# Kernel optimization log

Measured on AMD Instinct MI355X. Metric: run time of the kernel, lower is better.

## Reference

```python
import jax, jax.numpy as jnp
import numpy as np

B, N, E, H = 4, 512, 256, 8
D = E // H


def setup_inputs() -> dict:
    key = jax.random.key(0)
    ks = jax.random.split(key, 14)
    s = 1.0 / np.sqrt(E)
    inp = {
        "query": jax.random.normal(ks[0], (B, N, E), jnp.float32),
        "attn_bias": jax.random.normal(ks[1], (B * H, N, N), jnp.float32),
        "delta_pos": jax.random.normal(ks[2], (B, N, N, 3), jnp.float32),
        "drop_edge_mask": jax.random.bernoulli(ks[3], 0.1, (N, N)),
        "Wq": jax.random.normal(ks[4], (E, E), jnp.float32) * s,
        "bq": jnp.zeros((E,), jnp.float32),
        "Wk": jax.random.normal(ks[5], (E, E), jnp.float32) * s,
        "bk": jnp.zeros((E,), jnp.float32),
        "Wv": jax.random.normal(ks[6], (E, E), jnp.float32) * s,
        "bv": jnp.zeros((E,), jnp.float32),
        "Wf1": jax.random.normal(ks[7], (1, E), jnp.float32) * s,
        "bf1": jnp.zeros((1,), jnp.float32),
        "Wf2": jax.random.normal(ks[8], (1, E), jnp.float32) * s,
        "bf2": jnp.zeros((1,), jnp.float32),
        "Wf3": jax.random.normal(ks[9], (1, E), jnp.float32) * s,
        "bf3": jnp.zeros((1,), jnp.float32),
        "drop_or_add": 1,
    }
    return inp


def reference(query, attn_bias, delta_pos, drop_edge_mask, Wq, bq, Wk, bk, Wv, bv,
              Wf1, bf1, Wf2, bf2, Wf3, bf3, drop_or_add):
    b, n, e = query.shape
    h = H
    d = e // h
    scaling = (e // h) ** (-0.5)

    def proj(W, bias):  # [b,n,e] -> [b,h,n,d]
        return (query @ W.T + bias).reshape(b, n, h, d).transpose(0, 2, 1, 3)

    q = proj(Wq, bq) * scaling
    k = proj(Wk, bk)
    v = proj(Wv, bv)

    attn = jnp.einsum('bhnd,bhmd->bhnm', q, k) + attn_bias.reshape(b, h, n, n)
    # dropout prob 0.1 in training; reference runs in eval mode (no dropout)
    probs = jax.nn.softmax(attn, axis=-1)  # [b,h,n,n]

    # outer product with 3D displacement: [b,h,n,n,3] -> [b,h,3,n,n]
    rot = probs[..., None] * delta_pos[:, None]
    rot = jnp.transpose(rot, (0, 1, 4, 2, 3))
    if drop_or_add:
        # in-place masked_fill_ in the torch code affects the final matmul
        rot = jnp.where(drop_edge_mask[None, None, None], 0.0, rot)
    # note: original code overwrites x with rot_attn_probs @ v after both
    # branches, so the 'add' branch result is discarded -- replicated here.

    # [b,h,3,n,n] @ [b,h,n,d] -> [b,n,3,h,d] -> [b,n,3,h*d]
    x = jnp.einsum('bhcnm,bhmd->bnchd', rot, v).reshape(b, n, 3, e)

    f1 = x[:, :, 0, :] @ Wf1.T + bf1
    f2 = x[:, :, 1, :] @ Wf2.T + bf2
    f3 = x[:, :, 2, :] @ Wf3.T + bf3
    return jnp.concatenate([f1, f2, f3], axis=-1).astype(jnp.float32)  # [b,n,3]
```

## Files before the change

### kernel.cpp

```cpp
#include <hip/hip_runtime.h>
#include <hip/hip_bf16.h>

#define BB 4
#define NN 512
#define EE 256
#define HH 8
#define DD 32
#define SCALING 0.17677669529663687f
#define PR 8
#define RR 4

__global__ __launch_bounds__(256) void proj_kernel(
    const float* __restrict__ query,
    const float* __restrict__ Wq, const float* __restrict__ bq,
    const float* __restrict__ Wk, const float* __restrict__ bk,
    const float* __restrict__ Wv, const float* __restrict__ bv,
    const float* __restrict__ Wf1, const float* __restrict__ Wf2,
    const float* __restrict__ Wf3,
    float* __restrict__ Q, float* __restrict__ Kt, float* __restrict__ vw)
{
    __shared__ alignas(16) float s[PR][EE];
    __shared__ alignas(16) float sv[PR][EE];
    const int which = blockIdx.y;
    const int row0 = blockIdx.x * PR;
    const int tid = threadIdx.x;

    {
        const float4* src = (const float4*)(query + row0 * EE);
        ((float4*)s)[tid]       = src[tid];
        ((float4*)s)[tid + 256] = src[tid + 256];
    }
    __syncthreads();

    const float* W  = (which == 0) ? Wq : (which == 1) ? Wk : Wv;
    const float* bb = (which == 0) ? bq : (which == 1) ? bk : bv;

    float acc[PR];
    #pragma unroll
    for (int r = 0; r < PR; ++r) acc[r] = 0.f;

    const float4* W4 = (const float4*)(W + tid * EE);
    for (int j = 0; j < EE / 4; ++j) {
        const float4 w = W4[j];
        #pragma unroll
        for (int r = 0; r < PR; ++r) {
            const float4 x = *(const float4*)&s[r][4 * j];
            acc[r] += x.x * w.x + x.y * w.y + x.z * w.z + x.w * w.w;
        }
    }
    const float bbv = bb[tid];

    if (which == 0) {
        #pragma unroll
        for (int r = 0; r < PR; ++r)
            Q[(row0 + r) * EE + tid] = (acc[r] + bbv) * SCALING;
    } else if (which == 1) {
        const int h = tid >> 5, d = tid & 31;
        #pragma unroll
        for (int r = 0; r < PR; ++r) {
            const int grow = row0 + r;
            const int b = grow >> 9, n = grow & 511;
            Kt[((size_t)(b * HH + h) * DD + d) * NN + n] = acc[r] + bbv;
        }
    } else {
        #pragma unroll
        for (int r = 0; r < PR; ++r) sv[r][tid] = acc[r] + bbv;
        __syncthreads();
        if (tid < PR * 24) {
            const int r = tid / 24;
            const int rem = tid % 24;
            const int hh = rem / 3;
            const int c = rem % 3;
            const float* Wf = (c == 0) ? Wf1 : (c == 1) ? Wf2 : Wf3;
            float a = 0.f;
            #pragma unroll
            for (int dd = 0; dd < DD; ++dd)
                a += sv[r][hh * DD + dd] * Wf[hh * DD + dd];
            const int grow = row0 + r;
            const int b = grow >> 9, m = grow & 511;
            vw[((b * HH + hh) * 3 + c) * NN + m] = a;
        }
    }
}

__global__ __launch_bounds__(512) void attn_fused_kernel(
    const float* __restrict__ Q, const float* __restrict__ Kt,
    const float* __restrict__ attn_bias, const float* __restrict__ vw,
    const float* __restrict__ delta_pos,
    const int* __restrict__ drop_edge_mask, const int* __restrict__ drop_or_add,
    const float* __restrict__ bf1, const float* __restrict__ bf2,
    const float* __restrict__ bf3, float* __restrict__ out)
{
    const int blk = blockIdx.x;
    const int b = blk >> 7;
    const int n0 = (blk & 127) * RR;
    const int m = threadIdx.x;
    const int wv = m >> 6, ln = m & 63;

    __shared__ float sdp[RR * 3 * NN];
    __shared__ float red[HH][RR][8];
    __shared__ float srcp[HH][RR];
    __shared__ float r3[RR][3][8];

    {
        const float* dpb = delta_pos + (size_t)(b * NN + n0) * NN * 3;
        #pragma unroll
        for (int i = 0; i < RR * 3; ++i)
            sdp[i * 512 + m] = dpb[i * 512 + m];
    }

    unsigned int ep[HH][RR / 2];

    #pragma unroll
    for (int h = 0; h < HH; ++h) {
        const float* kp = Kt + ((size_t)(b * HH + h) * DD) * NN + m;
        const size_t bias_base = ((size_t)(b * HH + h) * NN + n0) * NN + m;
        const float* qb = Q + (b * NN + n0) * EE + h * DD;

        float l[RR];
        #pragma unroll
        for (int r = 0; r < RR; ++r)
            l[r] = attn_bias[bias_base + (size_t)r * NN];

        #pragma unroll
        for (int dc = 0; dc < DD; dc += 8) {
            float k8[8];
            #pragma unroll
            for (int i = 0; i < 8; ++i)
                k8[i] = kp[(size_t)(dc + i) * NN];
            #pragma unroll
            for (int i = 0; i < 8; ++i) {
                #pragma unroll
                for (int r = 0; r < RR; ++r)
                    l[r] += qb[r * EE + dc + i] * k8[i];
            }
        }

        float e[RR];
        #pragma unroll
        for (int r = 0; r < RR; ++r)
            e[r] = __expf(l[r]);

        #pragma unroll
        for (int r = 0; r < RR; ++r) {
            float x = e[r];
            #pragma unroll
            for (int off = 32; off; off >>= 1)
                x += __shfl_xor(x, off, 64);
            if (ln == 0) red[h][r][wv] = x;
        }

        #pragma unroll
        for (int rp = 0; rp < RR / 2; ++rp) {
            const unsigned int u0 =
                (unsigned int)__bfloat16_as_ushort(__float2bfloat16(e[2 * rp]));
            const unsigned int u1 =
                (unsigned int)__bfloat16_as_ushort(__float2bfloat16(e[2 * rp + 1]));
            ep[h][rp] = u0 | (u1 << 16);
        }
    }
    __syncthreads();

    if (m < HH * RR) {
        const int h = m >> 2, r = m & 3;
        float s = 0.f;
        #pragma unroll
        for (int w = 0; w < 8; ++w) s += red[h][r][w];
        srcp[h][r] = __builtin_amdgcn_rcpf(s);
    }
    __syncthreads();

    float A0[RR], A1[RR], A2[RR];
    #pragma unroll
    for (int r = 0; r < RR; ++r) { A0[r] = 0.f; A1[r] = 0.f; A2[r] = 0.f; }

    #pragma unroll
    for (int h = 0; h < HH; ++h) {
        const float* vwp = vw + (b * HH + h) * 3 * NN + m;
        const float vw0 = vwp[0], vw1 = vwp[NN], vw2 = vwp[2 * NN];
        #pragma unroll
        for (int rp = 0; rp < RR / 2; ++rp) {
            const unsigned int u = ep[h][rp];
            const float e0 = __uint_as_float(u << 16) * srcp[h][2 * rp];
            const float e1 = __uint_as_float(u & 0xffff0000u) * srcp[h][2 * rp + 1];
            A0[2 * rp] += e0 * vw0;  A0[2 * rp + 1] += e1 * vw0;
            A1[2 * rp] += e0 * vw1;  A1[2 * rp + 1] += e1 * vw1;
            A2[2 * rp] += e0 * vw2;  A2[2 * rp + 1] += e1 * vw2;
        }
    }

    const int doa = drop_or_add[0];
    #pragma unroll
    for (int r = 0; r < RR; ++r) {
        const float mk =
            (doa != 0 && drop_edge_mask[(n0 + r) * NN + m] != 0) ? 0.f : 1.f;
        const float* dp = &sdp[r * 3 * NN + 3 * m];
        float v0 = A0[r] * dp[0] * mk;
        float v1 = A1[r] * dp[1] * mk;
        float v2 = A2[r] * dp[2] * mk;
        #pragma unroll
        for (int off = 32; off; off >>= 1) {
            v0 += __shfl_xor(v0, off, 64);
            v1 += __shfl_xor(v1, off, 64);
            v2 += __shfl_xor(v2, off, 64);
        }
        if (ln == 0) {
            r3[r][0][wv] = v0; r3[r][1][wv] = v1; r3[r][2][wv] = v2;
        }
    }
    __syncthreads();

    if (m < RR * 3) {
        const int r = m / 3, c = m % 3;
        float s = 0.f;
        #pragma unroll
        for (int w = 0; w < 8; ++w) s += r3[r][c][w];
        const float bias = (c == 0) ? bf1[0] : (c == 1) ? bf2[0] : bf3[0];
        out[(b * NN + n0 + r) * 3 + c] = s + bias;
    }
}

extern "C" void kernel_launch(void* const* d_in, const int* in_sizes, int n_in,
                              void* d_out, int out_size, void* d_ws, size_t ws_size,
                              hipStream_t stream)
{
    const float* query          = (const float*)d_in[0];
    const float* attn_bias      = (const float*)d_in[1];
    const float* delta_pos      = (const float*)d_in[2];
    const int*   drop_edge_mask = (const int*)d_in[3];
    const float* Wq  = (const float*)d_in[4];
    const float* bq  = (const float*)d_in[5];
    const float* Wk  = (const float*)d_in[6];
    const float* bk  = (const float*)d_in[7];
    const float* Wv  = (const float*)d_in[8];
    const float* bv  = (const float*)d_in[9];
    const float* Wf1 = (const float*)d_in[10];
    const float* bf1 = (const float*)d_in[11];
    const float* Wf2 = (const float*)d_in[12];
    const float* bf2 = (const float*)d_in[13];
    const float* Wf3 = (const float*)d_in[14];
    const float* bf3 = (const float*)d_in[15];
    const int*   drop_or_add = (const int*)d_in[16];

    float* ws = (float*)d_ws;
    float* Q   = ws;
    float* Kt  = ws + 524288;
    float* vw  = ws + 1048576;

    proj_kernel<<<dim3(BB * NN / PR, 3), 256, 0, stream>>>(
        query, Wq, bq, Wk, bk, Wv, bv, Wf1, Wf2, Wf3, Q, Kt, vw);
    attn_fused_kernel<<<BB * NN / RR, 512, 0, stream>>>(
        Q, Kt, attn_bias, vw, delta_pos, drop_edge_mask, drop_or_add,
        bf1, bf2, bf3, (float*)d_out);
}
```

Before: 65.32 us.

## Assign one head per wavefront in fused attention kernel

Remaps the fused attention kernel so each of the 8 wavefronts owns one head and loops over key chunks of 64, instead of each thread owning a key column and looping over all heads. The softmax denominator is now reduced within a single wavefront via shuffles, which removes a shared-memory reduction and one block barrier. The mask and delta_pos multiply moves inside the per-head loop, so mask loads and LDS reads are repeated per head (8x more mask global reads), and the cross-head sum is done at the end through shared memory.

```diff
diff --git a/kernel.cpp b/kernel.cpp
--- a/kernel.cpp
+++ b/kernel.cpp
@@ -9,6 +9,7 @@
 #define SCALING 0.17677669529663687f
 #define PR 8
 #define RR 4
+#define CH (NN / 64)
 
 __global__ __launch_bounds__(256) void proj_kernel(
     const float* __restrict__ query,
@@ -94,40 +95,41 @@
     const int blk = blockIdx.x;
     const int b = blk >> 7;
     const int n0 = (blk & 127) * RR;
-    const int m = threadIdx.x;
-    const int wv = m >> 6, ln = m & 63;
+    const int tid = threadIdx.x;
+    const int ln = tid & 63;
+    const int h = __builtin_amdgcn_readfirstlane(tid >> 6);
 
     __shared__ float sdp[RR * 3 * NN];
-    __shared__ float red[HH][RR][8];
-    __shared__ float srcp[HH][RR];
-    __shared__ float r3[RR][3][8];
+    __shared__ float r3[HH][RR * 3];
 
     {
         const float* dpb = delta_pos + (size_t)(b * NN + n0) * NN * 3;
         #pragma unroll
         for (int i = 0; i < RR * 3; ++i)
-            sdp[i * 512 + m] = dpb[i * 512 + m];
-    }
-
-    unsigned int ep[HH][RR / 2];
-
-    #pragma unroll
-    for (int h = 0; h < HH; ++h) {
-        const float* kp = Kt + ((size_t)(b * HH + h) * DD) * NN + m;
-        const size_t bias_base = ((size_t)(b * HH + h) * NN + n0) * NN + m;
-        const float* qb = Q + (b * NN + n0) * EE + h * DD;
-
+            sdp[i * 512 + tid] = dpb[i * 512 + tid];
+    }
+
+    const float* kp    = Kt + (size_t)(b * HH + h) * DD * NN;
+    const float* qb    = Q + (b * NN + n0) * EE + h * DD;
+    const float* biasb = attn_bias + ((size_t)(b * HH + h) * NN + n0) * NN;
+
+    unsigned int ep[CH][RR / 2];
+    float S[RR] = {0.f, 0.f, 0.f, 0.f};
+
+    #pragma unroll
+    for (int c = 0; c < CH; ++c) {
+        const int m = c * 64 + ln;
         float l[RR];
         #pragma unroll
         for (int r = 0; r < RR; ++r)
-            l[r] = attn_bias[bias_base + (size_t)r * NN];
+            l[r] = biasb[(size_t)r * NN + m];
 
         #pragma unroll
         for (int dc = 0; dc < DD; dc += 8) {
             float k8[8];
             #pragma unroll
             for (int i = 0; i < 8; ++i)
-                k8[i] = kp[(size_t)(dc + i) * NN];
+                k8[i] = kp[(size_t)(dc + i) * NN + m];
             #pragma unroll
             for (int i = 0; i < 8; ++i) {
                 #pragma unroll
@@ -136,87 +138,82 @@
             }
         }
 
-        float e[RR];
-        #pragma unroll
-        for (int r = 0; r < RR; ++r)
-            e[r] = __expf(l[r]);
-
+        #pragma unroll
+        for (int rp = 0; rp < RR / 2; ++rp) {
+            const float e0 = __expf(l[2 * rp]);
+            const float e1 = __expf(l[2 * rp + 1]);
+            S[2 * rp]     += e0;
+            S[2 * rp + 1] += e1;
+            ep[c][rp] =
+                (unsigned)__bfloat16_as_ushort(__float2bfloat16(e0)) |
+                ((unsigned)__bfloat16_as_ushort(__float2bfloat16(e1)) << 16);
+        }
+    }
+
+    float srcp[RR];
+    #pragma unroll
+    for (int r = 0; r < RR; ++r) {
+        float x = S[r];
+        #pragma unroll
+        for (int off = 32; off; off >>= 1)
+            x += __shfl_xor(x, off, 64);
+        srcp[r] = __builtin_amdgcn_rcpf(x);
+    }
+
+    __syncthreads();
+
+    const int doa = drop_or_add[0];
+    float A[RR][3];
+    #pragma unroll
+    for (int r = 0; r < RR; ++r) { A[r][0] = 0.f; A[r][1] = 0.f; A[r][2] = 0.f; }
+
+    const float* vwb = vw + (size_t)(b * HH + h) * 3 * NN;
+    #pragma unroll
+    for (int c = 0; c < CH; ++c) {
+        const int m = c * 64 + ln;
+        const float v0 = vwb[m], v1 = vwb[NN + m], v2 = vwb[2 * NN + m];
         #pragma unroll
         for (int r = 0; r < RR; ++r) {
-            float x = e[r];
+            const unsigned u = ep[c][r >> 1];
+            const float e = (r & 1) ? __uint_as_float(u & 0xffff0000u)
+                                    : __uint_as_float(u << 16);
+            const float mk =
+                (doa != 0 && drop_edge_mask[(n0 + r) * NN + m] != 0) ? 0.f : 1.f;
+            const float t = e * srcp[r] * mk;
+            A[r][0] += t * v0 * sdp[r * 1536 + 3 * m + 0];
+            A[r][1] += t * v1 * sdp[r * 1536 + 3 * m + 1];
+            A[r][2] += t * v2 * sdp[r * 1536 + 3 * m + 2];
+        }
+    }
+
+    #pragma unroll
+    for (int r = 0; r < RR; ++r) {
+        #pragma unroll
+        for (int c3 = 0; c3 < 3; ++c3) {
+            float x = A[r][c3];
             #pragma unroll
             for (int off = 32; off; off >>= 1)
                 x += __shfl_xor(x, off, 64);
-            if (ln == 0) red[h][r][wv] = x;
-        }
-
-        #pragma unroll
-        for (int rp = 0; rp < RR / 2; ++rp) {
-            const unsigned int u0 =
-                (unsigned int)__bfloat16_as_ushort(__float2bfloat16(e[2 * rp]));
-            const unsigned int u1 =
-                (unsigned int)__bfloat16_as_ushort(__float2bfloat16(e[2 * rp + 1]));
-            ep[h][rp] = u0 | (u1 << 16);
+            A[r][c3] = x;
+        }
+    }
+    if (ln == 0) {
+        #pragma unroll
+        for (int r = 0; r < RR; ++r) {
+            #pragma unroll
+            for (int c3 = 0; c3 < 3; ++c3)
+                r3[h][r * 3 + c3] = A[r][c3];
         }
     }
     __syncthreads();
 
-    if (m < HH * RR) {
-        const int h = m >> 2, r = m & 3;
+    if (tid < RR * 3) {
         float s = 0.f;
         #pragma unroll
-        for (int w = 0; w < 8; ++w) s += red[h][r][w];
-        srcp[h][r] = __builtin_amdgcn_rcpf(s);
-    }
-    __syncthreads();
-
-    float A0[RR], A1[RR], A2[RR];
-    #pragma unroll
-    for (int r = 0; r < RR; ++r) { A0[r] = 0.f; A1[r] = 0.f; A2[r] = 0.f; }
-
-    #pragma unroll
-    for (int h = 0; h < HH; ++h) {
-        const float* vwp = vw + (b * HH + h) * 3 * NN + m;
-        const float vw0 = vwp[0], vw1 = vwp[NN], vw2 = vwp[2 * NN];
-        #pragma unroll
-        for (int rp = 0; rp < RR / 2; ++rp) {
-            const unsigned int u = ep[h][rp];
-            const float e0 = __uint_as_float(u << 16) * srcp[h][2 * rp];
-            const float e1 = __uint_as_float(u & 0xffff0000u) * srcp[h][2 * rp + 1];
-            A0[2 * rp] += e0 * vw0;  A0[2 * rp + 1] += e1 * vw0;
-            A1[2 * rp] += e0 * vw1;  A1[2 * rp + 1] += e1 * vw1;
-            A2[2 * rp] += e0 * vw2;  A2[2 * rp + 1] += e1 * vw2;
-        }
-    }
-
-    const int doa = drop_or_add[0];
-    #pragma unroll
-    for (int r = 0; r < RR; ++r) {
-        const float mk =
-            (doa != 0 && drop_edge_mask[(n0 + r) * NN + m] != 0) ? 0.f : 1.f;
-        const float* dp = &sdp[r * 3 * NN + 3 * m];
-        float v0 = A0[r] * dp[0] * mk;
-        float v1 = A1[r] * dp[1] * mk;
-        float v2 = A2[r] * dp[2] * mk;
-        #pragma unroll
-        for (int off = 32; off; off >>= 1) {
-            v0 += __shfl_xor(v0, off, 64);
-            v1 += __shfl_xor(v1, off, 64);
-            v2 += __shfl_xor(v2, off, 64);
-        }
-        if (ln == 0) {
-            r3[r][0][wv] = v0; r3[r][1][wv] = v1; r3[r][2][wv] = v2;
-        }
-    }
-    __syncthreads();
-
-    if (m < RR * 3) {
-        const int r = m / 3, c = m % 3;
-        float s = 0.f;
-        #pragma unroll
-        for (int w = 0; w < 8; ++w) s += r3[r][c][w];
-        const float bias = (c == 0) ? bf1[0] : (c == 1) ? bf2[0] : bf3[0];
-        out[(b * NN + n0 + r) * 3 + c] = s + bias;
+        for (int hh = 0; hh < HH; ++hh) s += r3[hh][tid];
+        const int r = tid / 3, cc = tid % 3;
+        const float bias = (cc == 0) ? bf1[0] : (cc == 1) ? bf2[0] : bf3[0];
+        out[(b * NN + n0 + r) * 3 + cc] = s + bias;
     }
 }
 
```

Result: slower. 80.26 us (+22.9%).
